# Kernel tuning notes

Hardware: AMD Instinct MI355X
Metric: run time of the kernel (lower is better)

Reference implementation:

```python
import jax, jax.numpy as jnp
import numpy as np

B, N, F_IN = 8, 256, 24
SLOPE = 0.01  # nn.LeakyReLU default negative_slope

def _leaky(x):
    return jnp.where(x >= 0, x, SLOPE * x)

def _adj(x, ws, bs):
    # AdjacencyMatrixPrediction (eval mode: dropout = identity, bn=False)
    # x: [B,N,F]; pairwise abs diff -> [B,N,N,F]; 1x1 convs == per-position matmuls
    h = jnp.abs(x[:, :, None, :] - x[:, None, :, :])
    for w, b in zip(ws[:4], bs[:4]):
        h = _leaky(h @ w + b)
    logits = (h @ ws[4] + bs[4])[..., 0]  # [B,N,N]
    n = x.shape[1]
    logits = logits - jnp.eye(n, dtype=logits.dtype) * 1e8  # mask diagonal
    return jax.nn.softmax(logits, axis=2)  # softmax over j (columns)

def _graph(a, x, w, b):
    # gmul with J2 operator = concat([I @ x, A @ x], -1), then Linear(J*F_in -> F_out)
    agg = jnp.concatenate([x, jnp.einsum('bij,bjf->bif', a, x)], axis=-1)
    return agg @ w.T + b

def setup_inputs():
    key = jax.random.key(0)
    ks = jax.random.split(key, 16)
    def mk(k, shape):
        return jax.random.normal(k, shape, jnp.float32) * 0.05
    ch0 = [24, 192, 192, 192, 96, 1]   # first AdjacencyMatrixPrediction conv chain
    ch1 = [72, 192, 192, 192, 96, 1]   # last AdjacencyMatrixPrediction (24 + 48 input)
    inp = {'x': jax.random.normal(ks[0], (B, N, F_IN), jnp.float32)}
    i = 1
    for pfx, ch in (('a0', ch0), ('a1', ch1)):
        for l in range(5):
            inp[f'{pfx}_w{l}'] = mk(ks[i], (ch[l], ch[l + 1])); i += 1
            inp[f'{pfx}_b{l}'] = jnp.zeros((ch[l + 1],), jnp.float32)
    inp['g0_w'] = mk(ks[i], (48, 48)); i += 1   # GraphModule(24 -> 48, J=2)
    inp['g0_b'] = jnp.zeros((48,), jnp.float32)
    inp['g1_w'] = mk(ks[i], (1, 144)); i += 1   # layer_last GraphModule(72 -> 1, J=2)
    inp['g1_b'] = jnp.zeros((1,), jnp.float32)
    return inp

def reference(x, a0_w0, a0_b0, a0_w1, a0_b1, a0_w2, a0_b2, a0_w3, a0_b3, a0_w4, a0_b4,
              a1_w0, a1_b0, a1_w1, a1_b1, a1_w2, a1_b2, a1_w3, a1_b3, a1_w4, a1_b4,
              g0_w, g0_b, g1_w, g1_b):
    a0 = _adj(x, [a0_w0, a0_w1, a0_w2, a0_w3, a0_w4], [a0_b0, a0_b1, a0_b2, a0_b3, a0_b4])
    x1 = _leaky(_graph(a0, x, g0_w, g0_b))
    xc = jnp.concatenate([x, x1], axis=-1)  # [B,N,72]
    a1 = _adj(xc, [a1_w0, a1_w1, a1_w2, a1_w3, a1_w4], [a1_b0, a1_b1, a1_b2, a1_b3, a1_b4])
    out = _graph(a1, xc, g1_w, g1_b)  # [B,N,1]
    # classifiers returned as [B,N,N,1] like the torch code
    return out, a0[..., None], a1[..., None]
```

## Files before the change

### kernel.cpp

```cpp
#include <hip/hip_runtime.h>

typedef __bf16 bf16x8 __attribute__((ext_vector_type(8)));
typedef float f32x4 __attribute__((ext_vector_type(4)));

__device__ __forceinline__ unsigned short f2b(float f) {
    union { float f; unsigned u; } c; c.f = f;
    unsigned u = c.u;
    return (unsigned short)((u + 0x7FFFu + ((u >> 16) & 1u)) >> 16);
}

__device__ __forceinline__ unsigned pack2(float v0, float v1) {
    union { __bf16 h[2]; unsigned u; } c;
    c.h[0] = (__bf16)v0; c.h[1] = (__bf16)v1;
    return c.u;
}

__device__ __forceinline__ void gload_lds16(const unsigned short* g, unsigned short* l) {
    __builtin_amdgcn_global_load_lds(
        (__attribute__((address_space(1))) unsigned int*)(g),
        (__attribute__((address_space(3))) unsigned int*)(l), 16, 0, 0);
}

template<int NLOADS>
__device__ __forceinline__ void stage_layer(const unsigned short* __restrict__ g,
                                            unsigned short* l, int wid, int lane)
{
#pragma unroll
    for (int k = 0; k < (NLOADS + 7) / 8; ++k) {
        const int idx = wid + k * 8;
        if ((NLOADS % 8 == 0) || idx < NLOADS)
            gload_lds16(g + idx * 512 + lane * 8, l + idx * 512);
    }
}

template<int CIN, int KN0>
__device__ __forceinline__ void build_frags0(const float* __restrict__ xi,
    const float* __restrict__ xj, int cl, int g, bf16x8 (&B0)[2][6])
{
#pragma unroll
    for (int s = 0; s < KN0; ++s) {
        const int f0 = s * 32 + 8 * g;
        const bool valid = f0 < CIN;
        f32x4 xa = {0.f,0.f,0.f,0.f}, xb = {0.f,0.f,0.f,0.f};
        if (valid) { xa = *(const f32x4*)(xi + f0); xb = *(const f32x4*)(xi + f0 + 4); }
#pragma unroll
        for (int t = 0; t < 2; ++t) {
            bf16x8 r;
            if (valid) {
                const float* pj = xj + (16 * t + cl) * CIN + f0;
                f32x4 ja = *(const f32x4*)pj, jb = *(const f32x4*)(pj + 4);
#pragma unroll
                for (int e = 0; e < 4; ++e) {
                    r[e]     = (__bf16)fabsf(xa[e] - ja[e]);
                    r[e + 4] = (__bf16)fabsf(xb[e] - jb[e]);
                }
            } else {
#pragma unroll
                for (int e = 0; e < 8; ++e) r[e] = (__bf16)0.f;
            }
            B0[t][s] = r;
        }
    }
}

template<int KN, int CB>
__device__ __forceinline__ void run_layer(const unsigned short* wlds,
    const float* __restrict__ bias, const bf16x8 (&Bc)[2][6], bf16x8 (&Bn)[2][6],
    int lane, int g)
{
#pragma unroll
    for (int cp = 0; cp < CB / 2; ++cp) {
        f32x4 acc[2][2];
#pragma unroll
        for (int cc = 0; cc < 2; ++cc) {
            f32x4 bv = *(const f32x4*)&bias[(2 * cp + cc) * 16 + 4 * g];
            acc[cc][0] = bv; acc[cc][1] = bv;
        }
#pragma unroll
        for (int s = 0; s < KN; ++s) {
#pragma unroll
            for (int cc = 0; cc < 2; ++cc) {
                bf16x8 w = *(const bf16x8*)&wlds[(((2 * cp + cc) * KN + s) * 64 + lane) * 8];
#pragma unroll
                for (int t = 0; t < 2; ++t)
                    acc[cc][t] = __builtin_amdgcn_mfma_f32_16x16x32_bf16(w, Bc[t][s], acc[cc][t], 0, 0, 0);
            }
        }
#pragma unroll
        for (int t = 0; t < 2; ++t) {
            union { unsigned w[4]; bf16x8 v; } outv;
#pragma unroll
            for (int cc = 0; cc < 2; ++cc)
#pragma unroll
                for (int m = 0; m < 2; ++m) {
                    float v0 = acc[cc][t][2 * m], v1 = acc[cc][t][2 * m + 1];
                    v0 = fmaxf(v0, 0.01f * v0);
                    v1 = fmaxf(v1, 0.01f * v1);
                    outv.w[cc * 2 + m] = pack2(v0, v1);
                }
            Bn[t][cp] = outv.v;
        }
    }
}

template<int CIN, int KN0>
__global__ __launch_bounds__(512, 2)
void adj_mlp_kernel(const float* __restrict__ src,
                    const unsigned short* __restrict__ wchain,
                    const unsigned short* __restrict__ w4f,
                    const float* __restrict__ b0, const float* __restrict__ b1,
                    const float* __restrict__ b2, const float* __restrict__ b3,
                    const float* __restrict__ b4,
                    float* __restrict__ logits)
{
    __shared__ unsigned short wbuf[2][36864];
    const int tid = threadIdx.x;
    const int wid = tid >> 6, lane = tid & 63;
    const int cl = lane & 15, g = lane >> 4;

    const int u = blockIdx.x * 8 + wid;
    const int b = u / 1152;
    const int r = u - b * 1152;
    const int tp = r >> 5;
    const int row_in = r & 31;
    int rg = 0, tt = tp;
#pragma unroll 8
    for (;;) { int cnt = 8 - rg; if (tt < cnt) break; tt -= cnt; ++rg; }
    const int cg = rg + tt;
    const int i = rg * 32 + row_in;
    const int j0 = cg * 32;
    const bool offdiag = (cg != rg);

    const float* xi = src + (b * 256 + i) * CIN;
    const float* xj = src + (b * 256 + j0) * CIN;

    stage_layer<12 * KN0>(wchain, wbuf[0], wid, lane);

    bf16x8 Ba[2][6], Bb[2][6];
    build_frags0<CIN, KN0>(xi, xj, cl, g, Ba);
    __syncthreads();

    stage_layer<72>(wchain + 12 * KN0 * 512, wbuf[1], wid, lane);
    run_layer<KN0, 12>(wbuf[0], b0, Ba, Bb, lane, g);
    __syncthreads();

    stage_layer<72>(wchain + 12 * KN0 * 512 + 36864, wbuf[0], wid, lane);
    run_layer<6, 12>(wbuf[1], b1, Bb, Ba, lane, g);
    __syncthreads();

    stage_layer<36>(wchain + 12 * KN0 * 512 + 73728, wbuf[1], wid, lane);
    run_layer<6, 12>(wbuf[0], b2, Ba, Bb, lane, g);
    __syncthreads();

    run_layer<6, 6>(wbuf[1], b3, Bb, Ba, lane, g);

    const float bv4 = b4[0];
#pragma unroll
    for (int t = 0; t < 2; ++t) {
        f32x4 acc = {bv4, bv4, bv4, bv4};
#pragma unroll
        for (int s = 0; s < 3; ++s) {
            bf16x8 w = *(const bf16x8*)(w4f + (s * 64 + lane) * 8);
            acc = __builtin_amdgcn_mfma_f32_16x16x32_bf16(w, Ba[t][s], acc, 0, 0, 0);
        }
        if (g == 0) {
            int j = j0 + 16 * t + cl;
            float lg = acc[0];
            if (j == i) lg -= 1e8f;
            logits[(b * 256 + i) * 256 + j] = lg;
            if (offdiag)
                logits[(b * 256 + j) * 256 + i] = lg;
        }
    }
}

struct PackPtrs { const float* w[10]; };

__global__ void pack_kernel(PackPtrs pp, unsigned short* __restrict__ dst)
{
    const int K_[10]   = {24, 192, 192, 192, 72, 192, 192, 192, 96, 96};
    const int KN_[10]  = {1, 6, 6, 6, 3, 6, 6, 6, 3, 3};
    const int NO_[10]  = {192, 192, 192, 96, 192, 192, 192, 96, 1, 1};
    const int OFF_[10] = {0, 6144, 43008, 79872, 98304, 116736, 153600, 190464, 208896, 210432};
    const int LEN_[10] = {6144, 36864, 36864, 18432, 18432, 36864, 36864, 18432, 1536, 1536};
    int t = blockIdx.x * 256 + threadIdx.x;
    int layer = 0, base = 0;
#pragma unroll
    for (int L = 0; L < 10; ++L)
        if (t >= base + LEN_[L]) { base += LEN_[L]; layer = L + 1; }
    if (layer >= 10) return;
    int u = t - base;
    int e = u & 7;
    int lane = (u >> 3) & 63;
    int gg = lane >> 4;
    int KN = KN_[layer];
    int fi = u >> 9;
    int s = fi % KN;
    int c = fi / KN;
    int k;
    if (layer == 0 || layer == 4)
        k = s * 32 + gg * 8 + e;
    else
        k = s * 32 + ((e >> 2) << 4) + (gg << 2) + (e & 3);
    int col = (c << 4) + (lane & 15);
    float v = 0.f;
    if (layer < 8) {
        if (k < K_[layer]) v = pp.w[layer][k * NO_[layer] + col];
    } else {
        if ((lane & 15) == 0) v = pp.w[layer][k];
    }
    dst[OFF_[layer] + u] = f2b(v);
}

template<int F>
__global__ __launch_bounds__(256)
void softmax_agg_kernel(float* __restrict__ amat, const float* __restrict__ src,
                        float* __restrict__ agg)
{
    __shared__ float pl[256];
    __shared__ float redm[4], reds[4];
    const int row = blockIdx.x;
    const int b = row >> 8;
    float* arow = amat + row * 256;
    const int t = threadIdx.x;
    const int lane = t & 63, wid = t >> 6;
    float v = arow[t];
    float m = v;
#pragma unroll
    for (int off = 32; off; off >>= 1) m = fmaxf(m, __shfl_xor(m, off));
    if (lane == 0) redm[wid] = m;
    __syncthreads();
    m = fmaxf(fmaxf(redm[0], redm[1]), fmaxf(redm[2], redm[3]));
    float e = __expf(v - m);
    float sum = e;
#pragma unroll
    for (int off = 32; off; off >>= 1) sum += __shfl_xor(sum, off);
    if (lane == 0) reds[wid] = sum;
    __syncthreads();
    sum = reds[0] + reds[1] + reds[2] + reds[3];
    float p = e / sum;
    arow[t] = p;
    pl[t] = p;
    __syncthreads();
    if (t < F) {
        const float* sb = src + (b * 256) * F + t;
        float acc = 0.f;
#pragma unroll 8
        for (int j = 0; j < 256; ++j)
            acc += pl[j] * sb[j * F];
        agg[row * F + t] = acc;
    }
}

__global__ __launch_bounds__(64)
void graph0_kernel(const float* __restrict__ x, const float* __restrict__ agg0,
                   const float* __restrict__ w, const float* __restrict__ bias,
                   float* __restrict__ xc)
{
    int row = blockIdx.x;
    int t = threadIdx.x;
    const float* xr = x + row * 24;
    const float* ar = agg0 + row * 24;
    if (t < 24) xc[row * 72 + t] = xr[t];
    if (t < 48) {
        float acc = bias[t];
#pragma unroll
        for (int f = 0; f < 24; ++f) acc += xr[f] * w[t * 48 + f];
#pragma unroll
        for (int f = 0; f < 24; ++f) acc += ar[f] * w[t * 48 + 24 + f];
        acc = acc >= 0.f ? acc : 0.01f * acc;
        xc[row * 72 + 24 + t] = acc;
    }
}

__global__ __launch_bounds__(64)
void graph1_kernel(const float* __restrict__ xc, const float* __restrict__ agg1,
                   const float* __restrict__ w, const float* __restrict__ bias,
                   float* __restrict__ out)
{
    int row = blockIdx.x;
    int t = threadIdx.x;
    float acc = 0.f;
    for (int idx = t; idx < 144; idx += 64) {
        float v = (idx < 72) ? xc[row * 72 + idx] : agg1[row * 72 + idx - 72];
        acc += v * w[idx];
    }
#pragma unroll
    for (int off = 32; off >= 1; off >>= 1) acc += __shfl_xor(acc, off);
    if (t == 0) out[row] = acc + bias[0];
}

extern "C" void kernel_launch(void* const* d_in, const int* in_sizes, int n_in,
                              void* d_out, int out_size, void* d_ws, size_t ws_size,
                              hipStream_t stream)
{
    const float* x = (const float*)d_in[0];
    float* out = (float*)d_out;
    float* a0 = out + 2048;
    float* a1 = a0 + 524288;

    char* ws = (char*)d_ws;
    unsigned short* packed = (unsigned short*)ws;
    float* xc   = (float*)(ws + 458752);
    float* agg0 = (float*)(ws + 1048576);
    float* agg1 = (float*)(ws + 1245184);

    PackPtrs pp;
    pp.w[0] = (const float*)d_in[1];
    pp.w[1] = (const float*)d_in[3];
    pp.w[2] = (const float*)d_in[5];
    pp.w[3] = (const float*)d_in[7];
    pp.w[4] = (const float*)d_in[11];
    pp.w[5] = (const float*)d_in[13];
    pp.w[6] = (const float*)d_in[15];
    pp.w[7] = (const float*)d_in[17];
    pp.w[8] = (const float*)d_in[9];
    pp.w[9] = (const float*)d_in[19];
    pack_kernel<<<828, 256, 0, stream>>>(pp, packed);

    adj_mlp_kernel<24, 1><<<1152, 512, 0, stream>>>(
        x, packed, packed + 208896,
        (const float*)d_in[2], (const float*)d_in[4], (const float*)d_in[6],
        (const float*)d_in[8], (const float*)d_in[10], a0);

    softmax_agg_kernel<24><<<2048, 256, 0, stream>>>(a0, x, agg0);

    graph0_kernel<<<2048, 64, 0, stream>>>(x, agg0,
        (const float*)d_in[21], (const float*)d_in[22], xc);

    adj_mlp_kernel<72, 3><<<1152, 512, 0, stream>>>(
        xc, packed + 98304, packed + 210432,
        (const float*)d_in[12], (const float*)d_in[14], (const float*)d_in[16],
        (const float*)d_in[18], (const float*)d_in[20], a1);

    softmax_agg_kernel<72><<<2048, 256, 0, stream>>>(a1, xc, agg1);

    graph1_kernel<<<2048, 64, 0, stream>>>(xc, agg1,
        (const float*)d_in[23], (const float*)d_in[24], out);
}
```

Measured before the change: 173.5 us.

## Stream MLP weights per channel-pair through small LDS double buffer with smaller blocks

Replaces whole-layer LDS staging (two 72 KB buffers) with per-output-channel-pair staging into two 12 KB buffers, with the load of the next pair overlapping compute on the current one. Blocks shrink from 8 to 4 waves and the grid doubles, so LDS use per block drops sharply and more blocks can be resident per CU. In exchange there are many more __syncthreads barriers (about 20 per block instead of 4), and each weight fragment is loaded by fewer waves, so there is less reuse per load.

```diff
diff --git a/kernel.cpp b/kernel.cpp
--- a/kernel.cpp
+++ b/kernel.cpp
@@ -21,14 +21,14 @@
         (__attribute__((address_space(3))) unsigned int*)(l), 16, 0, 0);
 }
 
-template<int NLOADS>
-__device__ __forceinline__ void stage_layer(const unsigned short* __restrict__ g,
+template<int NFRAGS>
+__device__ __forceinline__ void stage_frags(const unsigned short* __restrict__ g,
                                             unsigned short* l, int wid, int lane)
 {
 #pragma unroll
-    for (int k = 0; k < (NLOADS + 7) / 8; ++k) {
-        const int idx = wid + k * 8;
-        if ((NLOADS % 8 == 0) || idx < NLOADS)
+    for (int k = 0; k < (NFRAGS + 3) / 4; ++k) {
+        const int idx = wid + k * 4;
+        if ((NFRAGS % 4 == 0) || idx < NFRAGS)
             gload_lds16(g + idx * 512 + lane * 8, l + idx * 512);
     }
 }
@@ -63,48 +63,50 @@
     }
 }
 
-template<int KN, int CB>
-__device__ __forceinline__ void run_layer(const unsigned short* wlds,
+template<int KN, int CP>
+__device__ __forceinline__ void run_cpair(const unsigned short* wlds,
     const float* __restrict__ bias, const bf16x8 (&Bc)[2][6], bf16x8 (&Bn)[2][6],
     int lane, int g)
 {
-#pragma unroll
-    for (int cp = 0; cp < CB / 2; ++cp) {
-        f32x4 acc[2][2];
+    f32x4 acc[2][2];
+#pragma unroll
+    for (int cc = 0; cc < 2; ++cc) {
+        f32x4 bv = *(const f32x4*)&bias[(2 * CP + cc) * 16 + 4 * g];
+        acc[cc][0] = bv; acc[cc][1] = bv;
+    }
+#pragma unroll
+    for (int s = 0; s < KN; ++s) {
 #pragma unroll
         for (int cc = 0; cc < 2; ++cc) {
-            f32x4 bv = *(const f32x4*)&bias[(2 * cp + cc) * 16 + 4 * g];
-            acc[cc][0] = bv; acc[cc][1] = bv;
+            bf16x8 w = *(const bf16x8*)&wlds[((cc * KN + s) * 64 + lane) * 8];
+#pragma unroll
+            for (int t = 0; t < 2; ++t)
+                acc[cc][t] = __builtin_amdgcn_mfma_f32_16x16x32_bf16(w, Bc[t][s], acc[cc][t], 0, 0, 0);
         }
-#pragma unroll
-        for (int s = 0; s < KN; ++s) {
-#pragma unroll
-            for (int cc = 0; cc < 2; ++cc) {
-                bf16x8 w = *(const bf16x8*)&wlds[(((2 * cp + cc) * KN + s) * 64 + lane) * 8];
-#pragma unroll
-                for (int t = 0; t < 2; ++t)
-                    acc[cc][t] = __builtin_amdgcn_mfma_f32_16x16x32_bf16(w, Bc[t][s], acc[cc][t], 0, 0, 0);
+    }
+#pragma unroll
+    for (int t = 0; t < 2; ++t) {
+        union { unsigned w[4]; bf16x8 v; } outv;
+#pragma unroll
+        for (int cc = 0; cc < 2; ++cc)
+#pragma unroll
+            for (int m = 0; m < 2; ++m) {
+                float v0 = acc[cc][t][2 * m], v1 = acc[cc][t][2 * m + 1];
+                v0 = fmaxf(v0, 0.01f * v0);
+                v1 = fmaxf(v1, 0.01f * v1);
+                outv.w[cc * 2 + m] = pack2(v0, v1);
             }
-        }
-#pragma unroll
-        for (int t = 0; t < 2; ++t) {
-            union { unsigned w[4]; bf16x8 v; } outv;
-#pragma unroll
-            for (int cc = 0; cc < 2; ++cc)
-#pragma unroll
-                for (int m = 0; m < 2; ++m) {
-                    float v0 = acc[cc][t][2 * m], v1 = acc[cc][t][2 * m + 1];
-                    v0 = fmaxf(v0, 0.01f * v0);
-                    v1 = fmaxf(v1, 0.01f * v1);
-                    outv.w[cc * 2 + m] = pack2(v0, v1);
-                }
-            Bn[t][cp] = outv.v;
-        }
-    }
-}
+        Bn[t][CP] = outv.v;
+    }
+}
+
+#define STEP(NF, OFF, ...) \
+    stage_frags<NF>(wchain + (OFF), nxt, wid, lane); \
+    __VA_ARGS__; \
+    __syncthreads(); { unsigned short* tswp_ = cur; cur = nxt; nxt = tswp_; }
 
 template<int CIN, int KN0>
-__global__ __launch_bounds__(512, 2)
+__global__ __launch_bounds__(256, 4)
 void adj_mlp_kernel(const float* __restrict__ src,
                     const unsigned short* __restrict__ wchain,
                     const unsigned short* __restrict__ w4f,
@@ -113,12 +115,12 @@
                     const float* __restrict__ b4,
                     float* __restrict__ logits)
 {
-    __shared__ unsigned short wbuf[2][36864];
+    __shared__ unsigned short wbuf0[6144], wbuf1[6144];
     const int tid = threadIdx.x;
     const int wid = tid >> 6, lane = tid & 63;
     const int cl = lane & 15, g = lane >> 4;
 
-    const int u = blockIdx.x * 8 + wid;
+    const int u = blockIdx.x * 4 + wid;
     const int b = u / 1152;
     const int r = u - b * 1152;
     const int tp = r >> 5;
@@ -134,25 +136,41 @@
     const float* xi = src + (b * 256 + i) * CIN;
     const float* xj = src + (b * 256 + j0) * CIN;
 
-    stage_layer<12 * KN0>(wchain, wbuf[0], wid, lane);
+    const int CPSZ0 = 2 * KN0 * 512;
+    const int B1 = 12 * KN0 * 512;
+    const int B2 = B1 + 36864;
+    const int B3 = B1 + 73728;
+    const int CPSZ = 6144;
+
+    stage_frags<2 * KN0>(wchain, wbuf0, wid, lane);
 
     bf16x8 Ba[2][6], Bb[2][6];
     build_frags0<CIN, KN0>(xi, xj, cl, g, Ba);
     __syncthreads();
-
-    stage_layer<72>(wchain + 12 * KN0 * 512, wbuf[1], wid, lane);
-    run_layer<KN0, 12>(wbuf[0], b0, Ba, Bb, lane, g);
-    __syncthreads();
-
-    stage_layer<72>(wchain + 12 * KN0 * 512 + 36864, wbuf[0], wid, lane);
-    run_layer<6, 12>(wbuf[1], b1, Bb, Ba, lane, g);
-    __syncthreads();
-
-    stage_layer<36>(wchain + 12 * KN0 * 512 + 73728, wbuf[1], wid, lane);
-    run_layer<6, 12>(wbuf[0], b2, Ba, Bb, lane, g);
-    __syncthreads();
-
-    run_layer<6, 6>(wbuf[1], b3, Bb, Ba, lane, g);
+    unsigned short* cur = wbuf0;
+    unsigned short* nxt = wbuf1;
+
+    STEP(2 * KN0, 1 * CPSZ0, run_cpair<KN0, 0>(cur, b0, Ba, Bb, lane, g))
+    STEP(2 * KN0, 2 * CPSZ0, run_cpair<KN0, 1>(cur, b0, Ba, Bb, lane, g))
+    STEP(2 * KN0, 3 * CPSZ0, run_cpair<KN0, 2>(cur, b0, Ba, Bb, lane, g))
+    STEP(2 * KN0, 4 * CPSZ0, run_cpair<KN0, 3>(cur, b0, Ba, Bb, lane, g))
+    STEP(2 * KN0, 5 * CPSZ0, run_cpair<KN0, 4>(cur, b0, Ba, Bb, lane, g))
+    STEP(12, B1,             run_cpair<KN0, 5>(cur, b0, Ba, Bb, lane, g))
+    STEP(12, B1 + 1 * CPSZ,  run_cpair<6, 0>(cur, b1, Bb, Ba, lane, g))
+    STEP(12, B1 + 2 * CPSZ,  run_cpair<6, 1>(cur, b1, Bb, Ba, lane, g))
+    STEP(12, B1 + 3 * CPSZ,  run_cpair<6, 2>(cur, b1, Bb, Ba, lane, g))
+    STEP(12, B1 + 4 * CPSZ,  run_cpair<6, 3>(cur, b1, Bb, Ba, lane, g))
+    STEP(12, B1 + 5 * CPSZ,  run_cpair<6, 4>(cur, b1, Bb, Ba, lane, g))
+    STEP(12, B2,             run_cpair<6, 5>(cur, b1, Bb, Ba, lane, g))
+    STEP(12, B2 + 1 * CPSZ,  run_cpair<6, 0>(cur, b2, Ba, Bb, lane, g))
+    STEP(12, B2 + 2 * CPSZ,  run_cpair<6, 1>(cur, b2, Ba, Bb, lane, g))
+    STEP(12, B2 + 3 * CPSZ,  run_cpair<6, 2>(cur, b2, Ba, Bb, lane, g))
+    STEP(12, B2 + 4 * CPSZ,  run_cpair<6, 3>(cur, b2, Ba, Bb, lane, g))
+    STEP(12, B2 + 5 * CPSZ,  run_cpair<6, 4>(cur, b2, Ba, Bb, lane, g))
+    STEP(12, B3,             run_cpair<6, 5>(cur, b2, Ba, Bb, lane, g))
+    STEP(12, B3 + 1 * CPSZ,  run_cpair<6, 0>(cur, b3, Bb, Ba, lane, g))
+    STEP(12, B3 + 2 * CPSZ,  run_cpair<6, 1>(cur, b3, Bb, Ba, lane, g))
+    run_cpair<6, 2>(cur, b3, Bb, Ba, lane, g);
 
     const float bv4 = b4[0];
 #pragma unroll
@@ -318,7 +336,7 @@
     pp.w[9] = (const float*)d_in[19];
     pack_kernel<<<828, 256, 0, stream>>>(pp, packed);
 
-    adj_mlp_kernel<24, 1><<<1152, 512, 0, stream>>>(
+    adj_mlp_kernel<24, 1><<<2304, 256, 0, stream>>>(
         x, packed, packed + 208896,
         (const float*)d_in[2], (const float*)d_in[4], (const float*)d_in[6],
         (const float*)d_in[8], (const float*)d_in[10], a0);
@@ -328,7 +346,7 @@
     graph0_kernel<<<2048, 64, 0, stream>>>(x, agg0,
         (const float*)d_in[21], (const float*)d_in[22], xc);
 
-    adj_mlp_kernel<72, 3><<<1152, 512, 0, stream>>>(
+    adj_mlp_kernel<72, 3><<<2304, 256, 0, stream>>>(
         xc, packed + 98304, packed + 210432,
         (const float*)d_in[12], (const float*)d_in[14], (const float*)d_in[16],
         (const float*)d_in[18], (const float*)d_in[20], a1);
```

Result: slower. 250.5 us (+44.3%).
